# Optimization experiments

Hardware: AMD Instinct MI355X
Metric: run time of the kernel (lower is better)

Reference implementation:

```python
import jax, jax.numpy as jnp
import numpy as np

NHEAD = 8  # matches init_kwargs

M_NODES = 20000
D_MODEL = 512
N_EDGES = 640000


def setup_inputs() -> dict:
    key = jax.random.key(0)
    ks = jax.random.split(key, 8)
    sc = 1.0 / np.sqrt(D_MODEL)
    return {
        "s": jax.random.normal(ks[0], (M_NODES, D_MODEL), dtype=jnp.float32),
        "edge_index": jax.random.randint(ks[1], (2, N_EDGES), 0, M_NODES, dtype=jnp.int64),
        "Wq": jax.random.normal(ks[2], (D_MODEL, D_MODEL), dtype=jnp.float32) * sc,
        "bq": jax.random.normal(ks[3], (D_MODEL,), dtype=jnp.float32) * sc,
        "Wkv": jax.random.normal(ks[4], (2 * D_MODEL, D_MODEL), dtype=jnp.float32) * sc,
        "bkv": jax.random.normal(ks[5], (2 * D_MODEL,), dtype=jnp.float32) * sc,
        "Wo": jax.random.normal(ks[6], (D_MODEL, D_MODEL), dtype=jnp.float32) * sc,
        "bo": jax.random.normal(ks[7], (D_MODEL,), dtype=jnp.float32) * sc,
    }


def reference(s, edge_index, Wq, bq, Wkv, bkv, Wo, bo):
    M, C = s.shape
    H = NHEAD
    Dh = C // H
    scale = 1.0 / np.sqrt(Dh).astype(np.float32)

    q = (s @ Wq.T + bq).reshape(M, H, Dh)            # [M,H,Dh]
    kv = (s @ Wkv.T + bkv).reshape(M, H, 2 * Dh)     # [M,H,2Dh]
    k, v = kv[..., :Dh], kv[..., Dh:]

    src, tgt = edge_index[0], edge_index[1]

    # per-edge attention logits [E,H]
    a = jnp.einsum('ehc,ehc->eh', q[tgt], k[src]) * scale

    # segment softmax over edges sharing the same target node
    a_max = jax.ops.segment_max(a, tgt, num_segments=M)        # [M,H]
    ex = jnp.exp(a - a_max[tgt])                               # [E,H]
    denom = jax.ops.segment_sum(ex, tgt, num_segments=M)      # [M,H]
    attn = ex / denom[tgt]                                     # [E,H]

    # weighted message aggregation: scatter-sum over target nodes
    o_msg = attn[..., None] * v[src]                           # [E,H,Dh]
    o = jax.ops.segment_sum(o_msg, tgt, num_segments=M)       # [M,H,Dh]
    o = o.reshape(M, C)
    return o @ Wo.T + bo
```

## Files before the change

kernel.cpp:

```cpp
#include <hip/hip_runtime.h>
#include <cmath>

#define MN 20000
#define DM 512
#define NE 640000
#define CAP 128

typedef short bf16x8 __attribute__((ext_vector_type(8)));
typedef float f32x4 __attribute__((ext_vector_type(4)));

__device__ __forceinline__ ushort f2b(float x) {
    unsigned u = __builtin_bit_cast(unsigned, x);
    u += 0x7FFF + ((u >> 16) & 1);
    return (ushort)(u >> 16);
}
__device__ __forceinline__ float b2f(ushort b) {
    return __builtin_bit_cast(float, (unsigned)b << 16);
}

__global__ void conv_bf16_k(const float* __restrict__ in, ushort* __restrict__ out, int n4) {
    int i = blockIdx.x * blockDim.x + threadIdx.x;
    if (i >= n4) return;
    float4 v = ((const float4*)in)[i];
    ushort4 o = { f2b(v.x), f2b(v.y), f2b(v.z), f2b(v.w) };
    ((ushort4*)out)[i] = o;
}

__device__ __forceinline__ const float* wc_src_row(int r, const float* Wq, const float* Wkv) {
    if (r < 512) return Wq + ((size_t)r << 9);
    if (r < 1024) { int h = (r - 512) >> 6, j = (r - 512) & 63;  return Wkv + ((size_t)(h * 128 + j) << 9); }
    { int h = (r - 1024) >> 6, j = (r - 1024) & 63; return Wkv + ((size_t)(h * 128 + 64 + j) << 9); }
}

__global__ void conv_wc_k(const float* __restrict__ Wq, const float* __restrict__ Wkv,
                          ushort* __restrict__ out) {
    int i = blockIdx.x * blockDim.x + threadIdx.x;
    if (i >= 1536 * 512 / 4) return;
    int e = i * 4;
    int row = e >> 9, col = e & 511;
    float4 v = *(const float4*)(wc_src_row(row, Wq, Wkv) + col);
    ushort4 o = { f2b(v.x), f2b(v.y), f2b(v.z), f2b(v.w) };
    ((ushort4*)out)[i] = o;
}

__global__ void bias_perm_k(const float* __restrict__ bq, const float* __restrict__ bkv,
                            float* __restrict__ bc) {
    int r = blockIdx.x * blockDim.x + threadIdx.x;
    if (r >= 1536) return;
    float v;
    if (r < 512) v = bq[r];
    else if (r < 1024) { int h = (r - 512) >> 6, j = (r - 512) & 63;  v = bkv[h * 128 + j]; }
    else               { int h = (r - 1024) >> 6, j = (r - 1024) & 63; v = bkv[h * 128 + 64 + j]; }
    bc[r] = v;
}

template<int SPLIT, bool OUTBF>
__global__ __launch_bounds__(256) void gemm_mfma(
    const ushort* __restrict__ Ah, const ushort* __restrict__ Al,
    const ushort* __restrict__ Bh, const ushort* __restrict__ Bl,
    const float* __restrict__ bias, void* __restrict__ Cout, int M, int N, int K)
{
    __shared__ ushort lds[4 * 4096];
    const int tid = threadIdx.x;
    const int row0 = blockIdx.x * 128, col0 = blockIdx.y * 128;
    const int wid = tid >> 6, l = tid & 63;
    const int wm = (wid >> 1) * 64, wn = (wid & 1) * 64;
    const int fr = l & 15, g = l >> 4;
    const int fcb = g << 4;

    f32x4 acc[4][4] = {};

    for (int k0 = 0; k0 < K; k0 += 32) {
        __syncthreads();
#pragma unroll
        for (int c = 0; c < 2; ++c) {
            const int lb  = c * 4096 + tid * 16;
            const int r   = lb >> 6;
            const int cbs = (lb & 63) ^ ((r & 6) << 3);
            const int ar  = min(row0 + r, M - 1);
            const int br  = col0 + r;
            const size_t aoff = (size_t)ar * K + k0 + (cbs >> 1);
            const size_t boff = (size_t)br * K + k0 + (cbs >> 1);
            __builtin_amdgcn_global_load_lds(
                (const __attribute__((address_space(1))) void*)(Ah + aoff),
                (__attribute__((address_space(3))) void*)&lds[0 * 4096 + (lb >> 1)], 16, 0, 0);
            __builtin_amdgcn_global_load_lds(
                (const __attribute__((address_space(1))) void*)(Bh + boff),
                (__attribute__((address_space(3))) void*)&lds[1 * 4096 + (lb >> 1)], 16, 0, 0);
            if (SPLIT == 3) {
                __builtin_amdgcn_global_load_lds(
                    (const __attribute__((address_space(1))) void*)(Al + aoff),
                    (__attribute__((address_space(3))) void*)&lds[2 * 4096 + (lb >> 1)], 16, 0, 0);
                __builtin_amdgcn_global_load_lds(
                    (const __attribute__((address_space(1))) void*)(Bl + boff),
                    (__attribute__((address_space(3))) void*)&lds[3 * 4096 + (lb >> 1)], 16, 0, 0);
            }
        }
        __syncthreads();

        bf16x8 ah[4], bh[4], al[4], bl[4];
#pragma unroll
        for (int m = 0; m < 4; ++m) {
            const int r  = wm + m * 16 + fr;
            const int cb = fcb ^ ((r & 6) << 3);
            ah[m] = *(const bf16x8*)&lds[0 * 4096 + r * 32 + (cb >> 1)];
            if (SPLIT == 3) al[m] = *(const bf16x8*)&lds[2 * 4096 + r * 32 + (cb >> 1)];
        }
#pragma unroll
        for (int n = 0; n < 4; ++n) {
            const int r  = wn + n * 16 + fr;
            const int cb = fcb ^ ((r & 6) << 3);
            bh[n] = *(const bf16x8*)&lds[1 * 4096 + r * 32 + (cb >> 1)];
            if (SPLIT == 3) bl[n] = *(const bf16x8*)&lds[3 * 4096 + r * 32 + (cb >> 1)];
        }
#pragma unroll
        for (int m = 0; m < 4; ++m)
#pragma unroll
            for (int n = 0; n < 4; ++n) {
                acc[m][n] = __builtin_amdgcn_mfma_f32_16x16x32_bf16(ah[m], bh[n], acc[m][n], 0, 0, 0);
                if (SPLIT == 3) {
                    acc[m][n] = __builtin_amdgcn_mfma_f32_16x16x32_bf16(ah[m], bl[n], acc[m][n], 0, 0, 0);
                    acc[m][n] = __builtin_amdgcn_mfma_f32_16x16x32_bf16(al[m], bh[n], acc[m][n], 0, 0, 0);
                }
            }
    }

#pragma unroll
    for (int n = 0; n < 4; ++n) {
        const int cg = col0 + wn + n * 16 + fr;
        const float bv = bias[cg];
#pragma unroll
        for (int m = 0; m < 4; ++m) {
#pragma unroll
            for (int j = 0; j < 4; ++j) {
                const int rg = row0 + wm + m * 16 + g * 4 + j;
                if (rg < M) {
                    const float v = acc[m][n][j] + bv;
                    if (OUTBF) ((ushort*)Cout)[(size_t)rg * N + cg] = f2b(v);
                    else       ((float*)Cout)[(size_t)rg * N + cg] = v;
                }
            }
        }
    }
}

__global__ void count_edges_k(const int* __restrict__ tgt, int* __restrict__ counts, int E)
{
    int e = blockIdx.x * blockDim.x + threadIdx.x;
    if (e < E) atomicAdd(&counts[tgt[e]], 1);
}

__global__ __launch_bounds__(1024) void scan_counts_k(
    const int* __restrict__ counts, int* __restrict__ indptr,
    int* __restrict__ dbase, int M)
{
    __shared__ int part[1024];
    __shared__ int hist[128];
    const int t  = threadIdx.x;
    if (t < 128) hist[t] = 0;
    __syncthreads();
    const int CH = (M + 1023) / 1024;
    const int base = t * CH;
    int sum = 0;
    for (int i = 0; i < CH; ++i) {
        int idx = base + i;
        if (idx < M) {
            int c = counts[idx];
            sum += c;
            atomicAdd(&hist[127 - min(c, 127)], 1);
        }
    }
    part[t] = sum;
    __syncthreads();
    for (int off = 1; off < 1024; off <<= 1) {
        int v = (t >= off) ? part[t - off] : 0;
        __syncthreads();
        part[t] += v;
        __syncthreads();
    }
    int excl = part[t] - sum;
    for (int i = 0; i < CH; ++i) {
        int idx = base + i;
        if (idx < M) { indptr[idx] = excl; excl += counts[idx]; }
    }
    if (t == 1023) indptr[M] = part[1023];
    __syncthreads();
    if (t == 0) {
        int run = 0;
        for (int b = 0; b < 128; ++b) { int v = hist[b]; dbase[b] = run; run += v; }
    }
}

__global__ void scatter_edges_k(const int* __restrict__ src, const int* __restrict__ tgt,
                                const int* __restrict__ indptr, int* __restrict__ cursor,
                                int* __restrict__ slot_off, int E)
{
    int e = blockIdx.x * blockDim.x + threadIdx.x;
    if (e < E) {
        int t   = tgt[e];
        int pos = atomicAdd(&cursor[t], 1);
        slot_off[indptr[t] + pos] = src[e] * 3072;
    }
}

__global__ void deg_scatter_k(const int* __restrict__ counts, const int* __restrict__ dbase,
                              int* __restrict__ dcur, int* __restrict__ perm, int M)
{
    int n = blockIdx.x * blockDim.x + threadIdx.x;
    if (n < M) {
        int b = 127 - min(counts[n], 127);
        int pos = atomicAdd(&dcur[b], 1);
        perm[dbase[b] + pos] = n;
    }
}

__global__ __launch_bounds__(256, 4) void attn6_k(
    const ushort* __restrict__ qkv, const int* __restrict__ indptr,
    const int* __restrict__ slot_off, const int* __restrict__ perm,
    ushort* __restrict__ obh)
{
    __shared__ int slots[4][CAP];
    const int w = threadIdx.x >> 6;
    const int l = threadIdx.x & 63;
    const int node = perm[blockIdx.x * 4 + w];
    const int beg = indptr[node], end = indptr[node + 1];
    const int d = end - beg;
    const int dc = min(d, CAP);

    for (int i = l; i < dc; i += 64) slots[w][i] = slot_off[beg + i];
    __syncthreads();

    const char* base = (const char*)qkv + (l << 4);

    float qf[8];
    {
        bf16x8 qv = *(const bf16x8*)((const char*)qkv + (size_t)node * 3072 + (l << 4));
#pragma unroll
        for (int j = 0; j < 8; ++j) qf[j] = b2f((ushort)qv[j]);
    }

    float acc[8] = {};
    float ssum = 0.f;

    int i = 0;
    for (; i + 8 <= dc; i += 8) {
        const int4 sa = *(const int4*)&slots[w][i];
        const int4 sb = *(const int4*)&slots[w][i + 4];
        const char* bp[8] = { base + sa.x, base + sa.y, base + sa.z, base + sa.w,
                              base + sb.x, base + sb.y, base + sb.z, base + sb.w };
        bf16x8 kk[8], vv[8];
#pragma unroll
        for (int u = 0; u < 8; ++u) {
            kk[u] = *(const bf16x8*)(bp[u] + 1024);
            vv[u] = *(const bf16x8*)(bp[u] + 2048);
        }
        float p[8];
#pragma unroll
        for (int u = 0; u < 8; ++u) {
            float pu = 0.f;
#pragma unroll
            for (int j = 0; j < 8; ++j) pu = fmaf(qf[j], b2f((ushort)kk[u][j]), pu);
            p[u] = pu;
        }
#pragma unroll
        for (int u = 0; u < 8; ++u) p[u] += __shfl_xor(p[u], 1);
#pragma unroll
        for (int u = 0; u < 8; ++u) p[u] += __shfl_xor(p[u], 2);
#pragma unroll
        for (int u = 0; u < 8; ++u) p[u] += __shfl_xor(p[u], 4);
        float wt[8];
#pragma unroll
        for (int u = 0; u < 8; ++u) { wt[u] = __expf(p[u] * 0.125f); ssum += wt[u]; }
#pragma unroll
        for (int u = 0; u < 8; ++u)
#pragma unroll
            for (int j = 0; j < 8; ++j) acc[j] = fmaf(wt[u], b2f((ushort)vv[u][j]), acc[j]);
    }
    for (; i < d; ++i) {
        const int so = (i < CAP) ? slots[w][i] : slot_off[beg + i];
        const char* b0 = base + so;
        bf16x8 k0 = *(const bf16x8*)(b0 + 1024);
        bf16x8 v0 = *(const bf16x8*)(b0 + 2048);
        float p0 = 0.f;
#pragma unroll
        for (int j = 0; j < 8; ++j) p0 = fmaf(qf[j], b2f((ushort)k0[j]), p0);
        p0 += __shfl_xor(p0, 1); p0 += __shfl_xor(p0, 2); p0 += __shfl_xor(p0, 4);
        const float w0 = __expf(p0 * 0.125f);
        ssum += w0;
#pragma unroll
        for (int j = 0; j < 8; ++j) acc[j] = fmaf(w0, b2f((ushort)v0[j]), acc[j]);
    }

    const float inv = (d > 0) ? 1.f / ssum : 0.f;
    ushort4 ph0, ph1;
    ph0.x = f2b(acc[0] * inv); ph0.y = f2b(acc[1] * inv);
    ph0.z = f2b(acc[2] * inv); ph0.w = f2b(acc[3] * inv);
    ph1.x = f2b(acc[4] * inv); ph1.y = f2b(acc[5] * inv);
    ph1.z = f2b(acc[6] * inv); ph1.w = f2b(acc[7] * inv);
    const size_t ob_off = (size_t)node * 512 + (l << 3);
    *(ushort4*)(obh + ob_off)     = ph0;
    *(ushort4*)(obh + ob_off + 4) = ph1;
}

extern "C" void kernel_launch(void* const* d_in, const int* in_sizes, int n_in,
                              void* d_out, int out_size, void* d_ws, size_t ws_size,
                              hipStream_t stream)
{
    const float* s   = (const float*)d_in[0];
    const int*   eix = (const int*)d_in[1];
    const float* Wq  = (const float*)d_in[2];
    const float* bq  = (const float*)d_in[3];
    const float* Wkv = (const float*)d_in[4];
    const float* bkv = (const float*)d_in[5];
    const float* Wo  = (const float*)d_in[6];
    const float* bo  = (const float*)d_in[7];
    float* out = (float*)d_out;

    char* ws = (char*)d_ws;
    auto take = [&](size_t bytes) { char* p = ws; ws += (bytes + 255) & ~(size_t)255; return p; };
    ushort* qkv_b = (ushort*)take((size_t)MN * 1536 * 2);
    ushort* s_b   = (ushort*)take((size_t)MN * 512 * 2);
    ushort* obh   = (ushort*)take((size_t)MN * 512 * 2);
    ushort* Wc_b  = (ushort*)take((size_t)1536 * 512 * 2);
    ushort* Wo_b  = (ushort*)take((size_t)512 * 512 * 2);
    float*  bc    = (float*)take(1536 * 4);
    int* counts   = (int*)take(MN * 4);
    int* cursor   = (int*)take(MN * 4);
    int* slot_off = (int*)take((size_t)NE * 4);
    int* indptr   = (int*)take((MN + 4) * 4);
    int* dbase    = (int*)take(128 * 4);
    int* dcur     = (int*)take(128 * 4);
    int* perm     = (int*)take(MN * 4);

    hipMemsetAsync(counts, 0, MN * 4, stream);
    hipMemsetAsync(cursor, 0, MN * 4, stream);
    hipMemsetAsync(dcur, 0, 128 * 4, stream);

    conv_bf16_k<<<(MN * 512 / 4 + 255) / 256, 256, 0, stream>>>(s, s_b, MN * 512 / 4);
    conv_wc_k<<<(1536 * 512 / 4 + 255) / 256, 256, 0, stream>>>(Wq, Wkv, Wc_b);
    bias_perm_k<<<6, 256, 0, stream>>>(bq, bkv, bc);
    conv_bf16_k<<<(512 * 512 / 4 + 255) / 256, 256, 0, stream>>>(Wo, Wo_b, 512 * 512 / 4);

    count_edges_k<<<NE / 256, 256, 0, stream>>>(eix + NE, counts, NE);
    scan_counts_k<<<1, 1024, 0, stream>>>(counts, indptr, dbase, MN);
    scatter_edges_k<<<NE / 256, 256, 0, stream>>>(eix, eix + NE, indptr, cursor, slot_off, NE);
    deg_scatter_k<<<(MN + 255) / 256, 256, 0, stream>>>(counts, dbase, dcur, perm, MN);

    dim3 g1((MN + 127) / 128, 1536 / 128);
    gemm_mfma<1, true><<<g1, 256, 0, stream>>>(s_b, s_b, Wc_b, Wc_b, bc, qkv_b, MN, 1536, DM);

    attn6_k<<<MN / 4, 256, 0, stream>>>(qkv_b, indptr, slot_off, perm, obh);

    dim3 g2((MN + 127) / 128, 512 / 128);
    gemm_mfma<1, false><<<g2, 256, 0, stream>>>(obh, obh, Wo_b, Wo_b, bo, out, MN, 512, DM);
}
```

Baseline: 434.8 us.

## Fuse prep kernels and hand-schedule gather loads in attention loop

Merges the four conversion and bias-permutation kernels into one launch, and folds the degree-bucket scatter into the edge scatter kernel. In the attention kernel, the K and V gathers are now issued as inline-asm global_load_dwordx4 with explicit s_waitcnt, so the score computation can start before the V loads land. Launch bounds drop from 4 to 3 waves per SIMD to allow more registers. The goal is fewer launches and better memory-latency hiding, at the cost of fragile inline asm and possibly lower occupancy.

```diff
diff --git a/kernel.cpp b/kernel.cpp
--- a/kernel.cpp
+++ b/kernel.cpp
@@ -8,6 +8,7 @@
 
 typedef short bf16x8 __attribute__((ext_vector_type(8)));
 typedef float f32x4 __attribute__((ext_vector_type(4)));
+typedef int   i32x4 __attribute__((ext_vector_type(4)));
 
 __device__ __forceinline__ ushort f2b(float x) {
     unsigned u = __builtin_bit_cast(unsigned, x);
@@ -18,13 +19,10 @@
     return __builtin_bit_cast(float, (unsigned)b << 16);
 }
 
-__global__ void conv_bf16_k(const float* __restrict__ in, ushort* __restrict__ out, int n4) {
-    int i = blockIdx.x * blockDim.x + threadIdx.x;
-    if (i >= n4) return;
-    float4 v = ((const float4*)in)[i];
-    ushort4 o = { f2b(v.x), f2b(v.y), f2b(v.z), f2b(v.w) };
-    ((ushort4*)out)[i] = o;
-}
+#define NS4   (MN * DM / 4)
+#define NWC4  (1536 * 512 / 4)
+#define NWO4  (512 * 512 / 4)
+#define NB4   (1536 / 4)
 
 __device__ __forceinline__ const float* wc_src_row(int r, const float* Wq, const float* Wkv) {
     if (r < 512) return Wq + ((size_t)r << 9);
@@ -32,26 +30,46 @@
     { int h = (r - 1024) >> 6, j = (r - 1024) & 63; return Wkv + ((size_t)(h * 128 + 64 + j) << 9); }
 }
 
-__global__ void conv_wc_k(const float* __restrict__ Wq, const float* __restrict__ Wkv,
-                          ushort* __restrict__ out) {
+__global__ void conv_all_k(const float* __restrict__ s, const float* __restrict__ Wq,
+                           const float* __restrict__ Wkv, const float* __restrict__ Wo,
+                           const float* __restrict__ bq, const float* __restrict__ bkv,
+                           ushort* __restrict__ s_b, ushort* __restrict__ Wc_b,
+                           ushort* __restrict__ Wo_b, float* __restrict__ bc)
+{
     int i = blockIdx.x * blockDim.x + threadIdx.x;
-    if (i >= 1536 * 512 / 4) return;
-    int e = i * 4;
-    int row = e >> 9, col = e & 511;
-    float4 v = *(const float4*)(wc_src_row(row, Wq, Wkv) + col);
-    ushort4 o = { f2b(v.x), f2b(v.y), f2b(v.z), f2b(v.w) };
-    ((ushort4*)out)[i] = o;
-}
-
-__global__ void bias_perm_k(const float* __restrict__ bq, const float* __restrict__ bkv,
-                            float* __restrict__ bc) {
-    int r = blockIdx.x * blockDim.x + threadIdx.x;
-    if (r >= 1536) return;
-    float v;
-    if (r < 512) v = bq[r];
-    else if (r < 1024) { int h = (r - 512) >> 6, j = (r - 512) & 63;  v = bkv[h * 128 + j]; }
-    else               { int h = (r - 1024) >> 6, j = (r - 1024) & 63; v = bkv[h * 128 + 64 + j]; }
-    bc[r] = v;
+    if (i < NS4) {
+        float4 v = ((const float4*)s)[i];
+        ushort4 o = { f2b(v.x), f2b(v.y), f2b(v.z), f2b(v.w) };
+        ((ushort4*)s_b)[i] = o;
+        return;
+    }
+    i -= NS4;
+    if (i < NWC4) {
+        int e = i * 4, row = e >> 9, col = e & 511;
+        float4 v = *(const float4*)(wc_src_row(row, Wq, Wkv) + col);
+        ushort4 o = { f2b(v.x), f2b(v.y), f2b(v.z), f2b(v.w) };
+        ((ushort4*)Wc_b)[i] = o;
+        return;
+    }
+    i -= NWC4;
+    if (i < NWO4) {
+        float4 v = ((const float4*)Wo)[i];
+        ushort4 o = { f2b(v.x), f2b(v.y), f2b(v.z), f2b(v.w) };
+        ((ushort4*)Wo_b)[i] = o;
+        return;
+    }
+    i -= NWO4;
+    if (i < NB4) {
+#pragma unroll
+        for (int u = 0; u < 4; ++u) {
+            int r = i * 4 + u;
+            float v;
+            if (r < 512) v = bq[r];
+            else if (r < 1024) { int h = (r - 512) >> 6, j = (r - 512) & 63;  v = bkv[h * 128 + j]; }
+            else               { int h = (r - 1024) >> 6, j = (r - 1024) & 63; v = bkv[h * 128 + 64 + j]; }
+            bc[r] = v;
+        }
+    }
 }
 
 template<int SPLIT, bool OUTBF>
@@ -191,9 +209,11 @@
     }
 }
 
-__global__ void scatter_edges_k(const int* __restrict__ src, const int* __restrict__ tgt,
+__global__ void scatter_fused_k(const int* __restrict__ src, const int* __restrict__ tgt,
                                 const int* __restrict__ indptr, int* __restrict__ cursor,
-                                int* __restrict__ slot_off, int E)
+                                int* __restrict__ slot_off, const int* __restrict__ counts,
+                                const int* __restrict__ dbase, int* __restrict__ dcur,
+                                int* __restrict__ perm, int E, int M)
 {
     int e = blockIdx.x * blockDim.x + threadIdx.x;
     if (e < E) {
@@ -201,20 +221,14 @@
         int pos = atomicAdd(&cursor[t], 1);
         slot_off[indptr[t] + pos] = src[e] * 3072;
     }
-}
-
-__global__ void deg_scatter_k(const int* __restrict__ counts, const int* __restrict__ dbase,
-                              int* __restrict__ dcur, int* __restrict__ perm, int M)
-{
-    int n = blockIdx.x * blockDim.x + threadIdx.x;
-    if (n < M) {
-        int b = 127 - min(counts[n], 127);
+    if (e < M) {
+        int b = 127 - min(counts[e], 127);
         int pos = atomicAdd(&dcur[b], 1);
-        perm[dbase[b] + pos] = n;
-    }
-}
-
-__global__ __launch_bounds__(256, 4) void attn6_k(
+        perm[dbase[b] + pos] = e;
+    }
+}
+
+__global__ __launch_bounds__(256, 3) void attn7_k(
     const ushort* __restrict__ qkv, const int* __restrict__ indptr,
     const int* __restrict__ slot_off, const int* __restrict__ perm,
     ushort* __restrict__ obh)
@@ -248,18 +262,26 @@
         const int4 sb = *(const int4*)&slots[w][i + 4];
         const char* bp[8] = { base + sa.x, base + sa.y, base + sa.z, base + sa.w,
                               base + sb.x, base + sb.y, base + sb.z, base + sb.w };
-        bf16x8 kk[8], vv[8];
+        i32x4 kr[8], vr[8];
+#pragma unroll
+        for (int u = 0; u < 8; ++u)
+            asm volatile("global_load_dwordx4 %0, %1, off offset:1024"
+                         : "=v"(kr[u]) : "v"(bp[u]));
+#pragma unroll
+        for (int u = 0; u < 8; ++u)
+            asm volatile("global_load_dwordx4 %0, %1, off offset:2048"
+                         : "=v"(vr[u]) : "v"(bp[u]));
+
+        asm volatile("s_waitcnt vmcnt(8)" ::: "memory");
+        __builtin_amdgcn_sched_barrier(0);
+
+        float p[8];
 #pragma unroll
         for (int u = 0; u < 8; ++u) {
-            kk[u] = *(const bf16x8*)(bp[u] + 1024);
-            vv[u] = *(const bf16x8*)(bp[u] + 2048);
-        }
-        float p[8];
-#pragma unroll
-        for (int u = 0; u < 8; ++u) {
+            const bf16x8 kv = __builtin_bit_cast(bf16x8, kr[u]);
             float pu = 0.f;
 #pragma unroll
-            for (int j = 0; j < 8; ++j) pu = fmaf(qf[j], b2f((ushort)kk[u][j]), pu);
+            for (int j = 0; j < 8; ++j) pu = fmaf(qf[j], b2f((ushort)kv[j]), pu);
             p[u] = pu;
         }
 #pragma unroll
@@ -271,10 +293,16 @@
         float wt[8];
 #pragma unroll
         for (int u = 0; u < 8; ++u) { wt[u] = __expf(p[u] * 0.125f); ssum += wt[u]; }
-#pragma unroll
-        for (int u = 0; u < 8; ++u)
-#pragma unroll
-            for (int j = 0; j < 8; ++j) acc[j] = fmaf(wt[u], b2f((ushort)vv[u][j]), acc[j]);
+
+        asm volatile("s_waitcnt vmcnt(0)" ::: "memory");
+        __builtin_amdgcn_sched_barrier(0);
+
+#pragma unroll
+        for (int u = 0; u < 8; ++u) {
+            const bf16x8 vv = __builtin_bit_cast(bf16x8, vr[u]);
+#pragma unroll
+            for (int j = 0; j < 8; ++j) acc[j] = fmaf(wt[u], b2f((ushort)vv[j]), acc[j]);
+        }
     }
     for (; i < d; ++i) {
         const int so = (i < CAP) ? slots[w][i] : slot_off[beg + i];
@@ -336,20 +364,19 @@
     hipMemsetAsync(cursor, 0, MN * 4, stream);
     hipMemsetAsync(dcur, 0, 128 * 4, stream);
 
-    conv_bf16_k<<<(MN * 512 / 4 + 255) / 256, 256, 0, stream>>>(s, s_b, MN * 512 / 4);
-    conv_wc_k<<<(1536 * 512 / 4 + 255) / 256, 256, 0, stream>>>(Wq, Wkv, Wc_b);
-    bias_perm_k<<<6, 256, 0, stream>>>(bq, bkv, bc);
-    conv_bf16_k<<<(512 * 512 / 4 + 255) / 256, 256, 0, stream>>>(Wo, Wo_b, 512 * 512 / 4);
+    const int convN = NS4 + NWC4 + NWO4 + NB4;
+    conv_all_k<<<(convN + 255) / 256, 256, 0, stream>>>(s, Wq, Wkv, Wo, bq, bkv,
+                                                        s_b, Wc_b, Wo_b, bc);
 
     count_edges_k<<<NE / 256, 256, 0, stream>>>(eix + NE, counts, NE);
     scan_counts_k<<<1, 1024, 0, stream>>>(counts, indptr, dbase, MN);
-    scatter_edges_k<<<NE / 256, 256, 0, stream>>>(eix, eix + NE, indptr, cursor, slot_off, NE);
-    deg_scatter_k<<<(MN + 255) / 256, 256, 0, stream>>>(counts, dbase, dcur, perm, MN);
+    scatter_fused_k<<<NE / 256, 256, 0, stream>>>(eix, eix + NE, indptr, cursor,
+                                                  slot_off, counts, dbase, dcur, perm, NE, MN);
 
     dim3 g1((MN + 127) / 128, 1536 / 128);
     gemm_mfma<1, true><<<g1, 256, 0, stream>>>(s_b, s_b, Wc_b, Wc_b, bc, qkv_b, MN, 1536, DM);
 
-    attn6_k<<<MN / 4, 256, 0, stream>>>(qkv_b, indptr, slot_off, perm, obh);
+    attn7_k<<<MN / 4, 256, 0, stream>>>(qkv_b, indptr, slot_off, perm, obh);
 
     dim3 g2((MN + 127) / 128, 512 / 128);
     gemm_mfma<1, false><<<g2, 256, 0, stream>>>(obh, obh, Wo_b, Wo_b, bo, out, MN, 512, DM);
```

New measurement: 428.9 us. Within noise of the previous version (-1.4%).
